# Kernel tuning notes

Measured on AMD Instinct MI355X. Metric: run time of the kernel, lower is better.

Reference implementation:

```python
import jax, jax.numpy as jnp
import numpy as np

EMB_DIM = 256
DICT_SIZE = 8192
EPSILON = 1e-05


def setup_inputs() -> dict:
    key = jax.random.key(0)
    k_x, k_e = jax.random.split(key)
    x = jax.random.normal(k_x, (32, EMB_DIM, 32, 32), dtype=jnp.float32)
    embed = jax.random.normal(k_e, (DICT_SIZE, EMB_DIM), dtype=jnp.float32)
    embed = embed / jnp.linalg.norm(embed, axis=1, keepdims=True)  # F.normalize p=2
    track_num = jnp.zeros((DICT_SIZE, 1), dtype=jnp.float32)
    track_enc = embed  # buffers initialized as embed.clone()
    return {"x": x, "embed": embed, "track_num": track_num, "track_enc": track_enc}


def reference(x, embed, track_num, track_enc):
    b, c, h, w = x.shape
    K = embed.shape[0]
    # flatten: transpose(1,-1) -> [b,w,h,c], reshape -> [N, c]
    flat = jnp.transpose(x, (0, 3, 2, 1)).reshape(-1, c)  # [N, D]

    # KNN (k=1, l2): squared distance is monotone in l2, argmin identical
    x2 = jnp.sum(flat * flat, axis=1, keepdims=True)          # [N,1]
    e2 = jnp.sum(embed * embed, axis=1)                        # [K]
    d2 = x2 - 2.0 * (flat @ embed.T) + e2[None, :]             # [N,K]
    ids = jnp.argmin(d2, axis=1)                               # [N] int

    vqs_flat = embed[ids]                                      # [N, D]

    # EMA update, first-time path: buffers copied from raw statistics
    counts = jax.ops.segment_sum(jnp.ones_like(flat[:, 0]), ids, num_segments=K)
    new_track_num = counts[:, None]                            # [K,1]
    new_track_enc = jax.ops.segment_sum(flat, ids, num_segments=K)  # onehot.T @ flatten
    factor = 1.0 + EPSILON * K / new_track_num.sum()
    new_embed = new_track_enc * factor / (new_track_num + EPSILON)

    # restore spatial layout: view(b,w,h,c).transpose(1,-1) -> [b,c,h,w]
    vqs = jnp.transpose(vqs_flat.reshape(b, w, h, c), (0, 3, 2, 1))
    ids_out = jnp.transpose(ids.reshape(b, w, h), (0, 2, 1))   # [b,h,w]

    st_out = x + jax.lax.stop_gradient(vqs - x)                # straight-through
    loss = jnp.mean((jax.lax.stop_gradient(vqs) - x) ** 2)     # mse(vqs.detach(), input)
    return st_out, loss, ids_out, new_embed, new_track_num, new_track_enc
```

## Files before the change

### kernel.cpp

```cpp
#include <hip/hip_runtime.h>

#define NR 32768
#define CD 256
#define KD 8192

typedef __attribute__((ext_vector_type(8))) _Float16 f16x8;
typedef __attribute__((ext_vector_type(4))) _Float16 f16x4;
typedef __attribute__((ext_vector_type(4))) float f32x4;

#define F_XH      0ull
#define F_XL      4194304ull
#define F_EH      8388608ull
#define F_EMBT    9437184ull
#define F_E2N     11534336ull
#define F_E2NP    11542528ull
#define F_IDS     11550720ull
#define F_FLAGCNT 11583488ull
#define F_LOSS    11583489ull
#define F_FLAGLST 11583490ull
#define F_COUNTS  11616258ull
#define F_CURSOR  11624450ull
#define F_OFFS    11632642ull
#define F_BUCKET  11640834ull
#define F_PBD     11673602ull
#define F_PBI     11689986ull

#define OUT_ST   0ull
#define OUT_LOSS 8388608ull
#define OUT_IDS  8388609ull
#define OUT_NEMB 8421377ull
#define OUT_NUM  10518529ull
#define OUT_ENC  10526721ull

__device__ __forceinline__ float np_pw128(const float* p) {
    float r0 = p[0], r1 = p[1], r2 = p[2], r3 = p[3];
    float r4 = p[4], r5 = p[5], r6 = p[6], r7 = p[7];
    for (int i = 8; i < 128; i += 8) {
        r0 += p[i + 0]; r1 += p[i + 1]; r2 += p[i + 2]; r3 += p[i + 3];
        r4 += p[i + 4]; r5 += p[i + 5]; r6 += p[i + 6]; r7 += p[i + 7];
    }
    return ((r0 + r1) + (r2 + r3)) + ((r4 + r5) + (r6 + r7));
}

__global__ void k_cvt_x(const float* __restrict__ x,
                        _Float16* __restrict__ xh, _Float16* __restrict__ xl) {
    __shared__ float t[32 * 529];
    const int bx = blockIdx.x;
    const int b = bx >> 4, cg = (bx >> 1) & 7, h0 = (bx & 1) * 16;
    const int tid = threadIdx.x;
    const float* src = x + ((size_t)(b * 256 + cg * 32)) * 1024 + h0 * 32;
    #pragma unroll 4
    for (int i = 0; i < 16; ++i) {
        const int e4 = i * 256 + tid;
        const int c = e4 >> 7, rem = e4 & 127;
        const int hh = rem >> 3, w4 = (rem & 7) * 4;
        const float4 v = *(const float4*)(src + (size_t)c * 1024 + hh * 32 + w4);
        float* dst = &t[c * 529 + hh * 33 + w4];
        dst[0] = v.x; dst[1] = v.y; dst[2] = v.z; dst[3] = v.w;
    }
    __syncthreads();
    const int nj = tid >> 3;
    const int c4 = (tid & 7) * 4;
    #pragma unroll 4
    for (int i = 0; i < 16; ++i) {
        const int ns = i * 32 + nj;
        const int w = ns >> 4, hh = ns & 15;
        f16x4 hv, lv;
        #pragma unroll
        for (int j = 0; j < 4; ++j) {
            const float v = t[(c4 + j) * 529 + hh * 33 + w];
            const _Float16 hi = (_Float16)v;
            hv[j] = hi;
            lv[j] = (_Float16)(v - (float)hi);
        }
        const size_t o = ((size_t)(b * 1024 + w * 32 + h0 + hh)) * 256 + cg * 32 + c4;
        *(f16x4*)&xh[o] = hv;
        *(f16x4*)&xl[o] = lv;
    }
}

__global__ void k_prep_e2(const float* __restrict__ embed, _Float16* __restrict__ eh,
                          float* __restrict__ e2n, float* __restrict__ e2np) {
    const int lane = threadIdx.x & 63;
    const int wv = threadIdx.x >> 6;
    #pragma unroll
    for (int i = 0; i < 8; ++i) {
        const int k = blockIdx.x * 32 + wv * 8 + i;
        const float4 v = *(const float4*)(embed + (size_t)k * CD + lane * 4);
        f16x4 h;
        h[0] = (_Float16)v.x; h[1] = (_Float16)v.y;
        h[2] = (_Float16)v.z; h[3] = (_Float16)v.w;
        *(f16x4*)&eh[(size_t)k * CD + lane * 4] = h;
        float s = v.x * v.x + v.y * v.y + v.z * v.z + v.w * v.w;
        #pragma unroll
        for (int off = 1; off < 64; off <<= 1) s += __shfl_xor(s, off);
        if (lane == 0) e2n[k] = -0.5f * s;
    }
    const int k = blockIdx.x * 32 + wv * 8 + (lane >> 3);
    const int j = lane & 7;
    float hsum[2];
    #pragma unroll
    for (int half = 0; half < 2; ++half) {
        float r = 0.f;
        for (int i = 0; i < 16; ++i) {
            float v = embed[(size_t)k * CD + half * 128 + j + i * 8];
            float sq = v * v;
            asm volatile("" : "+v"(sq));
            r += sq;
        }
        float s = r + __shfl_xor(r, 1);
        s = s + __shfl_xor(s, 2);
        s = s + __shfl_xor(s, 4);
        hsum[half] = s;
    }
    if (j == 0) e2np[k] = hsum[0] + hsum[1];
}

__global__ void k_epose(const float* __restrict__ embed, float* __restrict__ embedT) {
    int kt = blockIdx.x >> 2, ct = blockIdx.x & 3;
    __shared__ float t[64][65];
    int tid = threadIdx.x;
    #pragma unroll
    for (int i = 0; i < 16; ++i) {
        int e = tid + i * 256; int r = e >> 6, c = e & 63;
        t[r][c] = embed[(size_t)(kt * 64 + r) * CD + ct * 64 + c];
    }
    __syncthreads();
    #pragma unroll
    for (int i = 0; i < 16; ++i) {
        int e = tid + i * 256; int c = e >> 6, r = e & 63;
        embedT[(size_t)(ct * 64 + c) * KD + kt * 64 + r] = t[r][c];
    }
}

#define LDSB 0
#define LDSA 65536
#define LDSM 131072
__global__ __launch_bounds__(512, 1) void k_mfma(
    const _Float16* __restrict__ xh, const _Float16* __restrict__ eh,
    const float* __restrict__ e2n, int* __restrict__ ids,
    int* __restrict__ flag_cnt, int* __restrict__ flag_list,
    int* __restrict__ counts)
{
    __shared__ char smem[131072 + 6144];
    const int tid = threadIdx.x;
    const int w = tid >> 6, l = tid & 63;
    const int wm = w & 3, wn = w >> 2;
    const int lr = l & 15, q = l >> 4;
    const int n0 = blockIdx.x * 128;

    #pragma unroll
    for (int i = 0; i < 8; ++i) {
        const int row = i * 16 + (tid >> 5);
        const int slot = tid & 31;
        const _Float16* src = xh + (size_t)(n0 + row) * 256 + ((slot ^ (row & 15)) * 8);
        __builtin_amdgcn_global_load_lds(
            (const __attribute__((address_space(1))) unsigned int*)src,
            (__attribute__((address_space(3))) unsigned int*)(smem + LDSB + row * 512 + slot * 16),
            16, 0, 0);
    }

    auto STAGE_A = [&](int s, int bufc) {
        if (s < 256) {
            const int bufo = LDSA + bufc * 16384;
            #pragma unroll
            for (int i = 0; i < 2; ++i) {
                const int code = i * 128 + (tid >> 2);
                const int slot = tid & 3;
                const _Float16* src = eh + (size_t)((s >> 3) * 256 + code) * 256
                                         + (s & 7) * 32 + ((slot ^ ((code >> 1) & 3)) * 8);
                __builtin_amdgcn_global_load_lds(
                    (const __attribute__((address_space(1))) unsigned int*)src,
                    (__attribute__((address_space(3))) unsigned int*)
                        (smem + bufo + code * 64 + slot * 16),
                    16, 0, 0);
            }
        } else {
            #pragma unroll
            for (int i = 0; i < 2; ++i) {
                __builtin_amdgcn_global_load_lds(
                    (const __attribute__((address_space(1))) unsigned int*)(eh + tid * 8),
                    (__attribute__((address_space(3))) unsigned int*)
                        (smem + LDSM + i * 1024 + (tid & 63) * 16),
                    16, 0, 0);
            }
        }
    };

    f32x4 e2c[4];
    #pragma unroll
    for (int m = 0; m < 4; ++m)
        e2c[m] = *(const f32x4*)(e2n + wm * 64 + m * 16 + q * 4);
    STAGE_A(0, 0); STAGE_A(1, 1); STAGE_A(2, 2);
    __builtin_amdgcn_sched_barrier(0);
    asm volatile("s_waitcnt vmcnt(4)" ::: "memory");
    __builtin_amdgcn_s_barrier();
    __builtin_amdgcn_sched_barrier(0);

    f32x4 acc[4][4];
    float m1[4], m2[4]; int i1[4];
    #pragma unroll
    for (int n = 0; n < 4; ++n) { m1[n] = -3.4e38f; m2[n] = -3.4e38f; i1[n] = 0; }

    int faoff[4];
    #pragma unroll
    for (int m = 0; m < 4; ++m) {
        const int code = wm * 64 + m * 16 + lr;
        faoff[m] = LDSA + code * 64 + ((q ^ ((code >> 1) & 3)) * 16);
    }
    int fboff[4], rx[4];
    #pragma unroll
    for (int n = 0; n < 4; ++n) {
        const int row = wn * 64 + n * 16 + lr;
        fboff[n] = LDSB + row * 512;
        rx[n] = row & 15;
    }

    #pragma unroll 1
    for (int cg = 0; cg < 32; ++cg) {
        #pragma unroll
        for (int cc = 0; cc < 8; ++cc) {
            const int s = cg * 8 + cc;
            if (cc == 6 && cg < 31) {
                #pragma unroll
                for (int m = 0; m < 4; ++m)
                    e2c[m] = *(const f32x4*)(e2n + (cg + 1) * 256 + wm * 64 + m * 16 + q * 4);
            }
            STAGE_A(s + 3, (cc + 3) & 3);
            const int bufo = LDSA + (cc & 3) * 16384;
            f16x8 fa[4], fb[4];
            #pragma unroll
            for (int m = 0; m < 4; ++m)
                fa[m] = *(const f16x8*)(smem + bufo + faoff[m] - LDSA);
            #pragma unroll
            for (int n = 0; n < 4; ++n) {
                const int g = cc * 4 + q;
                fb[n] = *(const f16x8*)(smem + fboff[n] + ((g ^ rx[n]) * 16));
            }
            if (cc == 0) {
                #pragma unroll
                for (int m = 0; m < 4; ++m)
                    #pragma unroll
                    for (int n = 0; n < 4; ++n)
                        acc[m][n] = __builtin_amdgcn_mfma_f32_16x16x32_f16(fa[m], fb[n], e2c[m], 0, 0, 0);
            } else {
                #pragma unroll
                for (int m = 0; m < 4; ++m)
                    #pragma unroll
                    for (int n = 0; n < 4; ++n)
                        acc[m][n] = __builtin_amdgcn_mfma_f32_16x16x32_f16(fa[m], fb[n], acc[m][n], 0, 0, 0);
            }
            if (cc == 7) {
                const int kb = cg * 256 + wm * 64 + q * 4;
                #pragma unroll
                for (int n = 0; n < 4; ++n)
                    #pragma unroll
                    for (int m = 0; m < 4; ++m)
                        #pragma unroll
                        for (int r = 0; r < 4; ++r) {
                            const float v = acc[m][n][r];
                            const bool g = v > m1[n];
                            m2[n] = fmaxf(m2[n], fminf(v, m1[n]));
                            m1[n] = fmaxf(m1[n], v);
                            i1[n] = g ? (kb + m * 16 + r) : i1[n];
                        }
            }
            __builtin_amdgcn_sched_barrier(0);
            asm volatile("s_waitcnt vmcnt(4)" ::: "memory");
            __builtin_amdgcn_s_barrier();
            __builtin_amdgcn_sched_barrier(0);
        }
    }

    #pragma unroll
    for (int off = 16; off < 64; off <<= 1) {
        #pragma unroll
        for (int n = 0; n < 4; ++n) {
            const float om1 = __shfl_xor(m1[n], off);
            const float om2 = __shfl_xor(m2[n], off);
            const int   oi  = __shfl_xor(i1[n], off);
            const bool g = om1 > m1[n];
            m2[n] = fmaxf(fminf(m1[n], om1), fmaxf(m2[n], om2));
            m1[n] = fmaxf(m1[n], om1);
            i1[n] = g ? oi : i1[n];
        }
    }
    float* sm1 = (float*)(smem + LDSM);
    float* sm2 = (float*)(smem + LDSM + 2048);
    int*   si1 = (int*)  (smem + LDSM + 4096);
    __syncthreads();
    if (q == 0) {
        #pragma unroll
        for (int n = 0; n < 4; ++n) {
            const int row = wn * 64 + n * 16 + lr;
            sm1[wm * 128 + row] = m1[n];
            sm2[wm * 128 + row] = m2[n];
            si1[wm * 128 + row] = i1[n];
        }
    }
    __syncthreads();
    if (tid < 128) {
        float a1 = sm1[tid], a2 = sm2[tid]; int ai = si1[tid];
        #pragma unroll
        for (int wq = 1; wq < 4; ++wq) {
            const float b1 = sm1[wq * 128 + tid], b2 = sm2[wq * 128 + tid];
            const int bi = si1[wq * 128 + tid];
            const bool g = b1 > a1;
            a2 = fmaxf(fminf(a1, b1), fmaxf(a2, b2));
            a1 = fmaxf(a1, b1);
            ai = g ? bi : ai;
        }
        const int n = n0 + tid;
        ids[n] = ai;
        atomicAdd(&counts[ai], 1);
        if (a1 - a2 < 2.5e-3f) {
            int p = atomicAdd(flag_cnt, 1);
            flag_list[p] = n;
        }
    }
}

#define RG 16
__global__ __launch_bounds__(256) void k_rescore(
    const float* __restrict__ x, const float* __restrict__ embedT,
    const float* __restrict__ e2np, const int* __restrict__ flag_cnt,
    const int* __restrict__ flag_list, float* __restrict__ pbd, int* __restrict__ pbi)
{
    __shared__ float rowl[RG][256];
    __shared__ float sq[RG][256];
    __shared__ float x2s[RG];
    __shared__ float bdA[256];
    __shared__ int   biA[256];
    const int tid = threadIdx.x;
    int cnt = *flag_cnt; if (cnt > 2048) cnt = 2048;
    const int ngroups = (cnt + RG - 1) / RG;
    const int kt = blockIdx.x & 7;
    for (int g = blockIdx.x >> 3; g < ngroups; g += 64) {
        #pragma unroll
        for (int i = 0; i < RG; ++i) {
            int f = g * RG + i;
            float v = 0.f;
            if (f < cnt) {
                int n = flag_list[f];
                int b = n >> 10, wq = (n >> 5) & 31, hq = n & 31;
                v = x[((size_t)(b * 256 + tid)) * 1024 + hq * 32 + wq];
            }
            rowl[i][tid] = v;
            sq[i][tid] = v * v;
        }
        __syncthreads();
        if (tid < RG) x2s[tid] = np_pw128(sq[tid]) + np_pw128(sq[tid] + 128);
        __syncthreads();

        float acc[RG][4];
        #pragma unroll
        for (int r = 0; r < RG; ++r)
            #pragma unroll
            for (int e = 0; e < 4; ++e) acc[r][e] = 0.f;
        for (int c = 0; c < 256; ++c) {
            const f32x4 bv = *(const f32x4*)&embedT[(size_t)c * KD + kt * 1024 + tid * 4];
            #pragma unroll
            for (int r = 0; r < RG; ++r) {
                const float av = rowl[r][c];
                acc[r][0] = fmaf(av, bv[0], acc[r][0]);
                acc[r][1] = fmaf(av, bv[1], acc[r][1]);
                acc[r][2] = fmaf(av, bv[2], acc[r][2]);
                acc[r][3] = fmaf(av, bv[3], acc[r][3]);
            }
        }
        #pragma unroll
        for (int r = 0; r < RG; ++r) {
            float bd = 3.4e38f; int bi = 0x7fffffff;
            #pragma unroll
            for (int e = 0; e < 4; ++e) {
                const int k = kt * 1024 + tid * 4 + e;
                const float d2 = (x2s[r] - 2.0f * acc[r][e]) + e2np[k];
                if (d2 < bd || (d2 == bd && k < bi)) { bd = d2; bi = k; }
            }
            bdA[tid] = bd; biA[tid] = bi;
            __syncthreads();
            for (int off = 128; off > 0; off >>= 1) {
                if (tid < off) {
                    float od = bdA[tid + off]; int oi = biA[tid + off];
                    if (od < bdA[tid] || (od == bdA[tid] && oi < biA[tid])) {
                        bdA[tid] = od; biA[tid] = oi;
                    }
                }
                __syncthreads();
            }
            if (tid == 0) {
                int f = g * RG + r;
                if (f < cnt) { pbd[f * 8 + kt] = bdA[0]; pbi[f * 8 + kt] = biA[0]; }
            }
            __syncthreads();
        }
    }
}

__global__ void k_flagmerge(const int* __restrict__ flag_cnt, const int* __restrict__ flag_list,
                            const float* __restrict__ pbd, const int* __restrict__ pbi,
                            int* __restrict__ ids, int* __restrict__ counts) {
    int cnt = *flag_cnt; if (cnt > 2048) cnt = 2048;
    int f = blockIdx.x * 256 + threadIdx.x;
    if (f >= cnt) return;
    float bd = pbd[f * 8]; int bi = pbi[f * 8];
    #pragma unroll
    for (int kt = 1; kt < 8; ++kt) {
        float d = pbd[f * 8 + kt]; int i = pbi[f * 8 + kt];
        if (d < bd || (d == bd && i < bi)) { bd = d; bi = i; }
    }
    const int n = flag_list[f];
    const int old = ids[n];
    if (bi != old) {
        ids[n] = bi;
        atomicAdd(&counts[old], -1);
        atomicAdd(&counts[bi], 1);
    }
}

__global__ __launch_bounds__(256) void k_output(
    const float* __restrict__ x, const float* __restrict__ embed,
    const int* __restrict__ ids, float* __restrict__ st,
    float* __restrict__ loss_ws)
{
    const int b = blockIdx.x >> 5, h = blockIdx.x & 31;
    const int tid = threadIdx.x;
    __shared__ int sid[32];
    __shared__ float vq[256 * 33];
    if (tid < 32) sid[tid] = ids[b * 1024 + tid * 32 + h];
    __syncthreads();
    #pragma unroll 4
    for (int w = 0; w < 32; ++w) {
        vq[tid * 33 + w] = embed[(size_t)sid[w] * CD + tid];
    }
    __syncthreads();
    float lsum = 0.f;
    const int j4 = (tid & 7) * 4;
    const int c0 = tid >> 3;
    const size_t base0 = (((size_t)b * 256) * 32 + h) * 32;
    #pragma unroll
    for (int it = 0; it < 8; ++it) {
        const int c = it * 32 + c0;
        const size_t a = base0 + (size_t)c * 1024 + j4;
        const float4 xv = *(const float4*)(x + a);
        float4 vv;
        vv.x = vq[c * 33 + j4 + 0];
        vv.y = vq[c * 33 + j4 + 1];
        vv.z = vq[c * 33 + j4 + 2];
        vv.w = vq[c * 33 + j4 + 3];
        *(float4*)(st + a) = vv;
        const float d0 = vv.x - xv.x, d1 = vv.y - xv.y;
        const float d2 = vv.z - xv.z, d3 = vv.w - xv.w;
        lsum = fmaf(d0, d0, lsum); lsum = fmaf(d1, d1, lsum);
        lsum = fmaf(d2, d2, lsum); lsum = fmaf(d3, d3, lsum);
    }
    #pragma unroll
    for (int off = 1; off < 64; off <<= 1) lsum += __shfl_xor(lsum, off);
    if ((tid & 63) == 0) atomicAdd(loss_ws, lsum);
}

__global__ void k_scan(const int* __restrict__ counts, int* __restrict__ offs,
                       float* __restrict__ track_num) {
    __shared__ int ps[257];
    const int tid = threadIdx.x;
    int loc[32]; int s = 0;
    const int base = tid * 32;
    #pragma unroll
    for (int j = 0; j < 32; ++j) { loc[j] = s; s += counts[base + j]; }
    ps[tid + 1] = s;
    if (tid == 0) ps[0] = 0;
    __syncthreads();
    if (tid == 0) for (int i = 1; i <= 256; ++i) ps[i] += ps[i - 1];
    __syncthreads();
    const int pre = ps[tid];
    #pragma unroll
    for (int j = 0; j < 32; ++j) {
        offs[base + j] = pre + loc[j];
        track_num[base + j] = (float)counts[base + j];
    }
}

__global__ void k_fill(const int* __restrict__ ids, const int* __restrict__ offs,
                       int* __restrict__ cursor, int* __restrict__ bucket,
                       float* __restrict__ ids_out) {
    int n = blockIdx.x * 256 + threadIdx.x;
    int id = ids[n];
    int p = atomicAdd(&cursor[id], 1);
    bucket[offs[id] + p] = n;
    int b = n >> 10, w = (n >> 5) & 31, h = n & 31;
    ids_out[b * 1024 + h * 32 + w] = (float)id;
}

__global__ void k_gather(const _Float16* __restrict__ xh, const _Float16* __restrict__ xl,
                         const int* __restrict__ offs, const int* __restrict__ counts,
                         const int* __restrict__ bucket, float* __restrict__ enc,
                         float* __restrict__ nemb, const float* __restrict__ loss_ws,
                         float* __restrict__ loss_out) {
    const int k = blockIdx.x, c = threadIdx.x;
    const int o = offs[k], cnt = counts[k];
    float s = 0.f;
    for (int i = 0; i < cnt; ++i) {
        int n = bucket[o + i];
        s += (float)xh[(size_t)n * CD + c] + (float)xl[(size_t)n * CD + c];
    }
    enc[(size_t)k * CD + c] = s;
    const float factor = 1.0f + (1e-5f * 8192.0f) / 32768.0f;
    nemb[(size_t)k * CD + c] = s * factor / ((float)cnt + 1e-5f);
    if (k == 0 && c == 0) loss_out[0] = loss_ws[0] * (1.0f / 8388608.0f);
}

extern "C" void kernel_launch(void* const* d_in, const int* in_sizes, int n_in,
                              void* d_out, int out_size, void* d_ws, size_t ws_size,
                              hipStream_t stream)
{
    const float* x     = (const float*)d_in[0];
    const float* embed = (const float*)d_in[1];
    float* out = (float*)d_out;
    float* ws  = (float*)d_ws;

    _Float16* xh = (_Float16*)(ws + F_XH);
    _Float16* xl = (_Float16*)(ws + F_XL);
    _Float16* eh = (_Float16*)(ws + F_EH);
    float* embedT    = ws + F_EMBT;
    float* e2n       = ws + F_E2N;
    float* e2np      = ws + F_E2NP;
    int*   ids       = (int*)(ws + F_IDS);
    int*   flag_cnt  = (int*)(ws + F_FLAGCNT);
    float* loss_ws   = ws + F_LOSS;
    int*   flag_list = (int*)(ws + F_FLAGLST);
    int*   counts    = (int*)(ws + F_COUNTS);
    int*   cursor    = (int*)(ws + F_CURSOR);
    int*   offs      = (int*)(ws + F_OFFS);
    int*   bucket    = (int*)(ws + F_BUCKET);
    float* pbd       = ws + F_PBD;
    int*   pbi       = (int*)(ws + F_PBI);

    hipMemsetAsync(ws + F_FLAGCNT, 0, 2 * sizeof(float), stream);
    hipMemsetAsync(ws + F_COUNTS, 0, 2 * 8192 * sizeof(float), stream);

    k_cvt_x    <<<512,  256, 0, stream>>>(x, xh, xl);
    k_prep_e2  <<<256,  256, 0, stream>>>(embed, eh, e2n, e2np);
    k_epose    <<<512,  256, 0, stream>>>(embed, embedT);
    k_mfma     <<<256,  512, 0, stream>>>(xh, eh, e2n, ids, flag_cnt, flag_list, counts);
    k_rescore  <<<512,  256, 0, stream>>>(x, embedT, e2np, flag_cnt, flag_list, pbd, pbi);
    k_flagmerge<<<8,    256, 0, stream>>>(flag_cnt, flag_list, pbd, pbi, ids, counts);
    k_output   <<<1024, 256, 0, stream>>>(x, embed, ids, out + OUT_ST, loss_ws);
    k_scan     <<<1,    256, 0, stream>>>(counts, offs, out + OUT_NUM);
    k_fill     <<<128,  256, 0, stream>>>(ids, offs, cursor, bucket, out + OUT_IDS);
    k_gather   <<<8192, 256, 0, stream>>>(xh, xl, offs, counts, bucket, out + OUT_ENC,
                                          out + OUT_NEMB, loss_ws, out + OUT_LOSS);
}
```

Measured before the change: 364.4 us.

## Halve k_mfma block tile to 64 rows and run two blocks per CU

The distance GEMM kernel now uses 256 threads per block with a 64-row x tile instead of 512 threads with 128 rows. The codebook staging ring drops from four buffers to three, prefetching two stages ahead, which frees LDS so two blocks fit per CU (launch_bounds 256,2). The grid doubles to 512 blocks. This is meant to raise occupancy and let the two blocks hide each other's barrier and load latency, but each codebook tile is now reused across only 64 rows, so the codebook is read from global memory twice as often.

```diff
diff --git a/kernel.cpp b/kernel.cpp
--- a/kernel.cpp
+++ b/kernel.cpp
@@ -134,24 +134,23 @@
 }
 
 #define LDSB 0
-#define LDSA 65536
-#define LDSM 131072
-__global__ __launch_bounds__(512, 1) void k_mfma(
+#define LDSA 32768
+#define LDSM 32768
+__global__ __launch_bounds__(256, 2) void k_mfma(
     const _Float16* __restrict__ xh, const _Float16* __restrict__ eh,
     const float* __restrict__ e2n, int* __restrict__ ids,
     int* __restrict__ flag_cnt, int* __restrict__ flag_list,
     int* __restrict__ counts)
 {
-    __shared__ char smem[131072 + 6144];
+    __shared__ __attribute__((aligned(16))) char smem[81920];
     const int tid = threadIdx.x;
-    const int w = tid >> 6, l = tid & 63;
-    const int wm = w & 3, wn = w >> 2;
+    const int wm = tid >> 6, l = tid & 63;
     const int lr = l & 15, q = l >> 4;
-    const int n0 = blockIdx.x * 128;
+    const int n0 = blockIdx.x * 64;
 
     #pragma unroll
     for (int i = 0; i < 8; ++i) {
-        const int row = i * 16 + (tid >> 5);
+        const int row = i * 8 + (tid >> 5);
         const int slot = tid & 31;
         const _Float16* src = xh + (size_t)(n0 + row) * 256 + ((slot ^ (row & 15)) * 8);
         __builtin_amdgcn_global_load_lds(
@@ -160,30 +159,19 @@
             16, 0, 0);
     }
 
-    auto STAGE_A = [&](int s, int bufc) {
-        if (s < 256) {
-            const int bufo = LDSA + bufc * 16384;
-            #pragma unroll
-            for (int i = 0; i < 2; ++i) {
-                const int code = i * 128 + (tid >> 2);
-                const int slot = tid & 3;
-                const _Float16* src = eh + (size_t)((s >> 3) * 256 + code) * 256
-                                         + (s & 7) * 32 + ((slot ^ ((code >> 1) & 3)) * 8);
-                __builtin_amdgcn_global_load_lds(
-                    (const __attribute__((address_space(1))) unsigned int*)src,
-                    (__attribute__((address_space(3))) unsigned int*)
-                        (smem + bufo + code * 64 + slot * 16),
-                    16, 0, 0);
-            }
-        } else {
-            #pragma unroll
-            for (int i = 0; i < 2; ++i) {
-                __builtin_amdgcn_global_load_lds(
-                    (const __attribute__((address_space(1))) unsigned int*)(eh + tid * 8),
-                    (__attribute__((address_space(3))) unsigned int*)
-                        (smem + LDSM + i * 1024 + (tid & 63) * 16),
-                    16, 0, 0);
-            }
+    auto STAGE_A = [&](int s) {
+        const int bufo = LDSA + (s % 3) * 16384;
+        #pragma unroll
+        for (int i = 0; i < 4; ++i) {
+            const int code = i * 64 + (tid >> 2);
+            const int slot = tid & 3;
+            const _Float16* src = eh + (size_t)((s >> 3) * 256 + code) * 256
+                                     + (s & 7) * 32 + ((slot ^ ((code >> 1) & 3)) * 8);
+            __builtin_amdgcn_global_load_lds(
+                (const __attribute__((address_space(1))) unsigned int*)src,
+                (__attribute__((address_space(3))) unsigned int*)
+                    (smem + bufo + code * 64 + slot * 16),
+                16, 0, 0);
         }
     };
 
@@ -191,7 +179,7 @@
     #pragma unroll
     for (int m = 0; m < 4; ++m)
         e2c[m] = *(const f32x4*)(e2n + wm * 64 + m * 16 + q * 4);
-    STAGE_A(0, 0); STAGE_A(1, 1); STAGE_A(2, 2);
+    STAGE_A(0); STAGE_A(1);
     __builtin_amdgcn_sched_barrier(0);
     asm volatile("s_waitcnt vmcnt(4)" ::: "memory");
     __builtin_amdgcn_s_barrier();
@@ -206,12 +194,12 @@
     #pragma unroll
     for (int m = 0; m < 4; ++m) {
         const int code = wm * 64 + m * 16 + lr;
-        faoff[m] = LDSA + code * 64 + ((q ^ ((code >> 1) & 3)) * 16);
+        faoff[m] = code * 64 + ((q ^ ((code >> 1) & 3)) * 16);
     }
     int fboff[4], rx[4];
     #pragma unroll
     for (int n = 0; n < 4; ++n) {
-        const int row = wn * 64 + n * 16 + lr;
+        const int row = n * 16 + lr;
         fboff[n] = LDSB + row * 512;
         rx[n] = row & 15;
     }
@@ -226,12 +214,12 @@
                 for (int m = 0; m < 4; ++m)
                     e2c[m] = *(const f32x4*)(e2n + (cg + 1) * 256 + wm * 64 + m * 16 + q * 4);
             }
-            STAGE_A(s + 3, (cc + 3) & 3);
-            const int bufo = LDSA + (cc & 3) * 16384;
+            STAGE_A(s + 2);
+            const int bufo = LDSA + (s % 3) * 16384;
             f16x8 fa[4], fb[4];
             #pragma unroll
             for (int m = 0; m < 4; ++m)
-                fa[m] = *(const f16x8*)(smem + bufo + faoff[m] - LDSA);
+                fa[m] = *(const f16x8*)(smem + bufo + faoff[m]);
             #pragma unroll
             for (int n = 0; n < 4; ++n) {
                 const int g = cc * 4 + q;
@@ -286,25 +274,25 @@
         }
     }
     float* sm1 = (float*)(smem + LDSM);
-    float* sm2 = (float*)(smem + LDSM + 2048);
-    int*   si1 = (int*)  (smem + LDSM + 4096);
+    float* sm2 = (float*)(smem + LDSM + 1024);
+    int*   si1 = (int*)  (smem + LDSM + 2048);
     __syncthreads();
     if (q == 0) {
         #pragma unroll
         for (int n = 0; n < 4; ++n) {
-            const int row = wn * 64 + n * 16 + lr;
-            sm1[wm * 128 + row] = m1[n];
-            sm2[wm * 128 + row] = m2[n];
-            si1[wm * 128 + row] = i1[n];
-        }
-    }
-    __syncthreads();
-    if (tid < 128) {
+            const int row = n * 16 + lr;
+            sm1[wm * 64 + row] = m1[n];
+            sm2[wm * 64 + row] = m2[n];
+            si1[wm * 64 + row] = i1[n];
+        }
+    }
+    __syncthreads();
+    if (tid < 64) {
         float a1 = sm1[tid], a2 = sm2[tid]; int ai = si1[tid];
         #pragma unroll
         for (int wq = 1; wq < 4; ++wq) {
-            const float b1 = sm1[wq * 128 + tid], b2 = sm2[wq * 128 + tid];
-            const int bi = si1[wq * 128 + tid];
+            const float b1 = sm1[wq * 64 + tid], b2 = sm2[wq * 64 + tid];
+            const int bi = si1[wq * 64 + tid];
             const bool g = b1 > a1;
             a2 = fmaxf(fminf(a1, b1), fmaxf(a2, b2));
             a1 = fmaxf(a1, b1);
@@ -541,7 +529,7 @@
     k_cvt_x    <<<512,  256, 0, stream>>>(x, xh, xl);
     k_prep_e2  <<<256,  256, 0, stream>>>(embed, eh, e2n, e2np);
     k_epose    <<<512,  256, 0, stream>>>(embed, embedT);
-    k_mfma     <<<256,  512, 0, stream>>>(xh, eh, e2n, ids, flag_cnt, flag_list, counts);
+    k_mfma     <<<512,  256, 0, stream>>>(xh, eh, e2n, ids, flag_cnt, flag_list, counts);
     k_rescore  <<<512,  256, 0, stream>>>(x, embedT, e2np, flag_cnt, flag_list, pbd, pbi);
     k_flagmerge<<<8,    256, 0, stream>>>(flag_cnt, flag_list, pbd, pbi, ids, counts);
     k_output   <<<1024, 256, 0, stream>>>(x, embed, ids, out + OUT_ST, loss_ws);
```

New measurement: 394.7 us. 1.08x slower.

## Give each wave private codebook staging buffers and drop per-step block barriers

Applied to the files above, without the earlier changes.

Each wave now stages its own 64-code slice of the fp16 codebook into a private triple-buffered LDS region, instead of sharing one block-wide quad-buffered stage. Because each wave only reads what it loaded itself, the per-step s_barrier is removed and replaced by a wave-local vmcnt wait, with prefetch depth reduced from three to two. The aim is to stop waves stalling on each other at every K-step. In exchange, the two waves that share a code slice both load it, doubling codebook traffic to L2. LDS use also grows to 160 KB, and the tail steps now prefetch rows past the end of the codebook.

```diff
diff --git a/kernel.cpp b/kernel.cpp
--- a/kernel.cpp
+++ b/kernel.cpp
@@ -135,19 +135,20 @@
 
 #define LDSB 0
 #define LDSA 65536
-#define LDSM 131072
+#define LDSM 65536
 __global__ __launch_bounds__(512, 1) void k_mfma(
     const _Float16* __restrict__ xh, const _Float16* __restrict__ eh,
     const float* __restrict__ e2n, int* __restrict__ ids,
     int* __restrict__ flag_cnt, int* __restrict__ flag_list,
     int* __restrict__ counts)
 {
-    __shared__ char smem[131072 + 6144];
+    __shared__ __attribute__((aligned(16))) char smem[163840];
     const int tid = threadIdx.x;
     const int w = tid >> 6, l = tid & 63;
     const int wm = w & 3, wn = w >> 2;
     const int lr = l & 15, q = l >> 4;
     const int n0 = blockIdx.x * 128;
+    const int AW = LDSA + w * 12288;
 
     #pragma unroll
     for (int i = 0; i < 8; ++i) {
@@ -160,30 +161,18 @@
             16, 0, 0);
     }
 
-    auto STAGE_A = [&](int s, int bufc) {
-        if (s < 256) {
-            const int bufo = LDSA + bufc * 16384;
-            #pragma unroll
-            for (int i = 0; i < 2; ++i) {
-                const int code = i * 128 + (tid >> 2);
-                const int slot = tid & 3;
-                const _Float16* src = eh + (size_t)((s >> 3) * 256 + code) * 256
-                                         + (s & 7) * 32 + ((slot ^ ((code >> 1) & 3)) * 8);
-                __builtin_amdgcn_global_load_lds(
-                    (const __attribute__((address_space(1))) unsigned int*)src,
-                    (__attribute__((address_space(3))) unsigned int*)
-                        (smem + bufo + code * 64 + slot * 16),
-                    16, 0, 0);
-            }
-        } else {
-            #pragma unroll
-            for (int i = 0; i < 2; ++i) {
-                __builtin_amdgcn_global_load_lds(
-                    (const __attribute__((address_space(1))) unsigned int*)(eh + tid * 8),
-                    (__attribute__((address_space(3))) unsigned int*)
-                        (smem + LDSM + i * 1024 + (tid & 63) * 16),
-                    16, 0, 0);
-            }
+    auto STAGE_A = [&](int s, int bufo) {
+        #pragma unroll
+        for (int i = 0; i < 4; ++i) {
+            const int code = i * 16 + (l >> 2);
+            const int slot = l & 3;
+            const _Float16* src = eh + (size_t)((s >> 3) * 256 + wm * 64 + code) * 256
+                                     + (s & 7) * 32 + ((slot ^ ((code >> 1) & 3)) * 8);
+            __builtin_amdgcn_global_load_lds(
+                (const __attribute__((address_space(1))) unsigned int*)src,
+                (__attribute__((address_space(3))) unsigned int*)
+                    (smem + AW + bufo + i * 1024 + l * 16),
+                16, 0, 0);
         }
     };
 
@@ -191,9 +180,10 @@
     #pragma unroll
     for (int m = 0; m < 4; ++m)
         e2c[m] = *(const f32x4*)(e2n + wm * 64 + m * 16 + q * 4);
-    STAGE_A(0, 0); STAGE_A(1, 1); STAGE_A(2, 2);
+    STAGE_A(0, 0);
+    STAGE_A(1, 4096);
     __builtin_amdgcn_sched_barrier(0);
-    asm volatile("s_waitcnt vmcnt(4)" ::: "memory");
+    asm volatile("s_waitcnt vmcnt(8)" ::: "memory");
     __builtin_amdgcn_s_barrier();
     __builtin_amdgcn_sched_barrier(0);
 
@@ -204,10 +194,8 @@
 
     int faoff[4];
     #pragma unroll
-    for (int m = 0; m < 4; ++m) {
-        const int code = wm * 64 + m * 16 + lr;
-        faoff[m] = LDSA + code * 64 + ((q ^ ((code >> 1) & 3)) * 16);
-    }
+    for (int m = 0; m < 4; ++m)
+        faoff[m] = AW + m * 1024 + lr * 64 + ((q ^ ((lr >> 1) & 3)) * 16);
     int fboff[4], rx[4];
     #pragma unroll
     for (int n = 0; n < 4; ++n) {
@@ -216,22 +204,28 @@
         rx[n] = row & 15;
     }
 
+    int cbo = 0, sbo = 8192;
+    #define ADVB(v) (v) = ((v) == 8192) ? 0 : (v) + 4096
+
     #pragma unroll 1
     for (int cg = 0; cg < 32; ++cg) {
         #pragma unroll
         for (int cc = 0; cc < 8; ++cc) {
             const int s = cg * 8 + cc;
+            __builtin_amdgcn_sched_barrier(0);
             if (cc == 6 && cg < 31) {
                 #pragma unroll
                 for (int m = 0; m < 4; ++m)
                     e2c[m] = *(const f32x4*)(e2n + (cg + 1) * 256 + wm * 64 + m * 16 + q * 4);
             }
-            STAGE_A(s + 3, (cc + 3) & 3);
-            const int bufo = LDSA + (cc & 3) * 16384;
+            STAGE_A(s + 2, sbo);
+            __builtin_amdgcn_sched_barrier(0);
+            asm volatile("s_waitcnt vmcnt(8)" ::: "memory");
+            __builtin_amdgcn_sched_barrier(0);
             f16x8 fa[4], fb[4];
             #pragma unroll
             for (int m = 0; m < 4; ++m)
-                fa[m] = *(const f16x8*)(smem + bufo + faoff[m] - LDSA);
+                fa[m] = *(const f16x8*)(smem + cbo + faoff[m]);
             #pragma unroll
             for (int n = 0; n < 4; ++n) {
                 const int g = cc * 4 + q;
@@ -265,12 +259,10 @@
                             i1[n] = g ? (kb + m * 16 + r) : i1[n];
                         }
             }
-            __builtin_amdgcn_sched_barrier(0);
-            asm volatile("s_waitcnt vmcnt(4)" ::: "memory");
-            __builtin_amdgcn_s_barrier();
-            __builtin_amdgcn_sched_barrier(0);
-        }
-    }
+            ADVB(cbo); ADVB(sbo);
+        }
+    }
+    #undef ADVB
 
     #pragma unroll
     for (int off = 16; off < 64; off <<= 1) {
```

New measurement: 390.1 us. +7.1%, slower.
